# Performance work log

Hardware: AMD Instinct MI355X
Metric: run time of the kernel (lower is better)

The kernel has to match this reference:

```python
import jax, jax.numpy as jnp
import numpy as np

B, M, P, A, T = 32, 128, 20, 32, 32
H = 32   # embed_size / local hidden
E = 64   # local_hidden_dim = 2*H, global attention embed dim


def setup_inputs() -> dict:
    key = jax.random.key(0)
    ks = jax.random.split(key, 10)
    def w(k, shape, fan):
        return jax.random.normal(k, shape, jnp.float32) / np.float32(np.sqrt(fan))
    z = lambda *s: jnp.zeros(s, jnp.float32)
    o = lambda *s: jnp.ones(s, jnp.float32)
    return {
        "map_states": jax.random.normal(ks[0], (B, M, P, 16), jnp.float32),
        "agent_states": jax.random.normal(ks[1], (B, A, T, 4), jnp.float32),
        "m_W1": w(ks[2], (16, H), 16), "m_b1": z(H), "m_g1": o(H), "m_be1": z(H),
        "m_W2": w(ks[3], (H, H), H),   "m_b2": z(H), "m_g2": o(H), "m_be2": z(H),
        "a_W1": w(ks[4], (4, H), 4),   "a_b1": z(H), "a_g1": o(H), "a_be1": z(H),
        "a_W2": w(ks[5], (H, H), H),   "a_b2": z(H), "a_g2": o(H), "a_be2": z(H),
        # stacked attention params: index 0 = a2m, 1 = agent(self), 2 = m2a
        "att_Wq": w(ks[6], (3, E, E), E), "att_bq": z(3, E),
        "att_Wk": w(ks[7], (3, E, E), E), "att_bk": z(3, E),
        "att_Wv": w(ks[8], (3, E, E), E), "att_bv": z(3, E),
        "att_Wo": w(ks[9], (3, E, E), E), "att_bo": z(3, E),
    }


def _mlp(x, W, b, g, be):
    # Linear -> LayerNorm -> ReLU
    h = x @ W + b
    mu = jnp.mean(h, axis=-1, keepdims=True)
    var = jnp.var(h, axis=-1, keepdims=True)
    h = (h - mu) / jnp.sqrt(var + 1e-5) * g + be
    return jax.nn.relu(h)


def _local_graph(x, p1, p2):
    # x: [B, N, P, F] -> [B, N, 2H]
    e = _mlp(_mlp(x, *p1), *p2)                       # [B,N,P,H]
    n = e.shape[2]
    # faithful "max excluding self": max_j (e[j] - 10000*[j==i])
    mask = -10000.0 * jnp.eye(n, dtype=e.dtype)       # [Pi,Pj]
    nb = jnp.max(e[:, :, None, :, :] + mask[None, None, :, :, None], axis=3)  # [B,N,P,H]
    e = jnp.concatenate([e, nb], axis=-1)             # [B,N,P,2H]
    return jnp.max(e, axis=2)                          # [B,N,2H]


def _mha(q, k, v, Wq, bq, Wk, bk, Wv, bv, Wo, bo):
    # single-head attention, batch_first
    d = q.shape[-1]
    Q = q @ Wq + bq
    K = k @ Wk + bk
    V = v @ Wv + bv
    scores = jnp.einsum('bqd,bkd->bqk', Q, K) / jnp.sqrt(jnp.asarray(d, Q.dtype))
    attn = jax.nn.softmax(scores, axis=-1)
    return jnp.einsum('bqk,bkd->bqd', attn, V) @ Wo + bo


def reference(map_states, agent_states,
              m_W1, m_b1, m_g1, m_be1, m_W2, m_b2, m_g2, m_be2,
              a_W1, a_b1, a_g1, a_be1, a_W2, a_b2, a_g2, a_be2,
              att_Wq, att_bq, att_Wk, att_bk, att_Wv, att_bv, att_Wo, att_bo):
    map_emb = _local_graph(map_states, (m_W1, m_b1, m_g1, m_be1), (m_W2, m_b2, m_g2, m_be2))      # [B,M,E]
    agent_emb = _local_graph(agent_states, (a_W1, a_b1, a_g1, a_be1), (a_W2, a_b2, a_g2, a_be2))  # [B,A,E]

    target = agent_emb[:, :1]                                       # [B,1,E]
    kv = jnp.concatenate([target, map_emb], axis=1)                 # [B,M+1,E]
    a2m = _mha(map_emb, kv, kv, att_Wq[0], att_bq[0], att_Wk[0], att_bk[0],
               att_Wv[0], att_bv[0], att_Wo[0], att_bo[0])
    map_emb = map_emb + a2m
    t_a = _mha(target, target, target, att_Wq[1], att_bq[1], att_Wk[1], att_bk[1],
               att_Wv[1], att_bv[1], att_Wo[1], att_bo[1])
    t_m2a = _mha(target, map_emb, map_emb, att_Wq[2], att_bq[2], att_Wk[2], att_bk[2],
                 att_Wv[2], att_bv[2], att_Wo[2], att_bo[2])
    target = t_a + t_m2a                                            # [B,1,E]
    # pack (target_agent_embedding, map_embedding) into one array [B, M+1, E]
    return jnp.concatenate([target, map_emb], axis=1)
```

## Files before the change

kernel.cpp:

```cpp
#include <hip/hip_runtime.h>

#define BB 32
#define MM 128
#define PP 20
#define AA 32
#define TT 32
#define HH 32
#define EE 64

__device__ __forceinline__ float4 matvec64(const float* __restrict__ W,
                                           const float* __restrict__ xrow,
                                           int s, int t)
{
    const float4* __restrict__ Wv = (const float4*)W;
    const float4* __restrict__ xv = (const float4*)xrow;
    float4 acc = make_float4(0.f, 0.f, 0.f, 0.f);
#pragma unroll
    for (int ii = 0; ii < 4; ++ii) {
        const float4 xx = xv[s * 4 + ii];
        const int ib = s * 16 + ii * 4;
        const float4 w0 = Wv[(ib + 0) * 16 + t];
        const float4 w1 = Wv[(ib + 1) * 16 + t];
        const float4 w2 = Wv[(ib + 2) * 16 + t];
        const float4 w3 = Wv[(ib + 3) * 16 + t];
        acc.x = fmaf(xx.x, w0.x, acc.x); acc.y = fmaf(xx.x, w0.y, acc.y);
        acc.z = fmaf(xx.x, w0.z, acc.z); acc.w = fmaf(xx.x, w0.w, acc.w);
        acc.x = fmaf(xx.y, w1.x, acc.x); acc.y = fmaf(xx.y, w1.y, acc.y);
        acc.z = fmaf(xx.y, w1.z, acc.z); acc.w = fmaf(xx.y, w1.w, acc.w);
        acc.x = fmaf(xx.z, w2.x, acc.x); acc.y = fmaf(xx.z, w2.y, acc.y);
        acc.z = fmaf(xx.z, w2.z, acc.z); acc.w = fmaf(xx.z, w2.w, acc.w);
        acc.x = fmaf(xx.w, w3.x, acc.x); acc.y = fmaf(xx.w, w3.y, acc.y);
        acc.z = fmaf(xx.w, w3.z, acc.z); acc.w = fmaf(xx.w, w3.w, acc.w);
    }
    acc.x += __shfl_xor(acc.x, 16); acc.y += __shfl_xor(acc.y, 16);
    acc.z += __shfl_xor(acc.z, 16); acc.w += __shfl_xor(acc.w, 16);
    acc.x += __shfl_xor(acc.x, 32); acc.y += __shfl_xor(acc.y, 32);
    acc.z += __shfl_xor(acc.z, 32); acc.w += __shfl_xor(acc.w, 32);
    return acc;
}

template <int IN, int P>
__device__ __forceinline__ void lg_qkv_body(const float* __restrict__ xg,
                                            const float* __restrict__ W1, const float* __restrict__ b1,
                                            const float* __restrict__ g1, const float* __restrict__ be1,
                                            const float* __restrict__ W2, const float* __restrict__ b2,
                                            const float* __restrict__ g2, const float* __restrict__ be2,
                                            float* __restrict__ embRow,
                                            const float* __restrict__ Wq, const float* __restrict__ bq,
                                            const float* __restrict__ Wk, const float* __restrict__ bk,
                                            const float* __restrict__ Wv, const float* __restrict__ bv,
                                            float* __restrict__ Qrow,
                                            float* __restrict__ Krow,
                                            float* __restrict__ Vrow)
{
    constexpr int NPASS = (P + 7) / 8;
    const int tid  = threadIdx.x;
    const int wave = tid >> 6;
    const int lane = tid & 63;
    const int sub  = tid >> 5;
    const int c    = tid & 31;

    __shared__ __align__(16) float aslot[8][32];
    __shared__ __align__(16) float wmax[4][32];
    __shared__ __align__(16) float xrow[EE];

    float4 xr[NPASS][IN / 4];
#pragma unroll
    for (int ps = 0; ps < NPASS; ++ps) {
        int p = ps * 8 + sub;
        if (p > P - 1) p = P - 1;
        const float4* xp4 = (const float4*)(xg + (long)p * IN);
#pragma unroll
        for (int j = 0; j < IN / 4; ++j) xr[ps][j] = xp4[j];
    }

    float w1c[IN];
#pragma unroll
    for (int k = 0; k < IN; ++k) w1c[k] = W1[k * HH + c];
    float w2c[HH];
#pragma unroll
    for (int k = 0; k < HH; ++k) w2c[k] = W2[k * HH + c];
    const float b1c = b1[c], g1c = g1[c], be1c = be1[c];
    const float b2c = b2[c], g2c = g2[c], be2c = be2[c];

    float cmax = -1e30f;

#pragma unroll
    for (int ps = 0; ps < NPASS; ++ps) {
        const bool valid = (ps * 8 + sub) < P;

        float ha = b1c, hb = 0.0f;
#pragma unroll
        for (int j = 0; j < IN / 4; ++j) {
            const float4 xx = xr[ps][j];
            ha = fmaf(xx.x, w1c[4 * j + 0], ha);
            hb = fmaf(xx.y, w1c[4 * j + 1], hb);
            ha = fmaf(xx.z, w1c[4 * j + 2], ha);
            hb = fmaf(xx.w, w1c[4 * j + 3], hb);
        }
        const float h = ha + hb;

        float s1 = h, s2 = h * h;
#pragma unroll
        for (int off = 16; off >= 1; off >>= 1) {
            s1 += __shfl_xor(s1, off, 32);
            s2 += __shfl_xor(s2, off, 32);
        }
        const float mu  = s1 * (1.0f / 32.0f);
        float var = s2 * (1.0f / 32.0f) - mu * mu;
        var = fmaxf(var, 0.0f);
        float a = (h - mu) * rsqrtf(var + 1e-5f) * g1c + be1c;
        a = fmaxf(a, 0.0f);

        aslot[sub][c] = a;
        const float4* av4 = (const float4*)aslot[sub];
        float h2a = b2c, h2b = 0.0f;
#pragma unroll
        for (int j = 0; j < 8; ++j) {
            const float4 aa = av4[j];
            h2a = fmaf(aa.x, w2c[4 * j + 0], h2a);
            h2b = fmaf(aa.y, w2c[4 * j + 1], h2b);
            h2a = fmaf(aa.z, w2c[4 * j + 2], h2a);
            h2b = fmaf(aa.w, w2c[4 * j + 3], h2b);
        }
        const float h2 = h2a + h2b;

        float t1 = h2, t2 = h2 * h2;
#pragma unroll
        for (int off = 16; off >= 1; off >>= 1) {
            t1 += __shfl_xor(t1, off, 32);
            t2 += __shfl_xor(t2, off, 32);
        }
        const float mu2  = t1 * (1.0f / 32.0f);
        float var2 = t2 * (1.0f / 32.0f) - mu2 * mu2;
        var2 = fmaxf(var2, 0.0f);
        float e = (h2 - mu2) * rsqrtf(var2 + 1e-5f) * g2c + be2c;
        e = fmaxf(e, 0.0f);

        if (valid) cmax = fmaxf(cmax, e);
    }

    cmax = fmaxf(cmax, __shfl_xor(cmax, 32));
    if (lane < 32) wmax[wave][lane] = cmax;
    __syncthreads();

    if (tid < 32) {
        float fin = fmaxf(fmaxf(wmax[0][tid], wmax[1][tid]),
                          fmaxf(wmax[2][tid], wmax[3][tid]));
        xrow[tid]      = fin;
        xrow[tid + 32] = fin;
        embRow[tid]      = fin;
        embRow[tid + 32] = fin;
    }
    __syncthreads();

    const int s = lane >> 4, t = lane & 15;
    if (wave == 0) {
        if (Qrow) {
            float4 q4 = matvec64(Wq, xrow, s, t);
            if (s == 0) {
                const float4 bq4 = ((const float4*)bq)[t];
                float4 qo;
                qo.x = (q4.x + bq4.x) * 0.125f;
                qo.y = (q4.y + bq4.y) * 0.125f;
                qo.z = (q4.z + bq4.z) * 0.125f;
                qo.w = (q4.w + bq4.w) * 0.125f;
                ((float4*)Qrow)[t] = qo;
            }
        }
    } else if (wave == 1) {
        float4 k4 = matvec64(Wk, xrow, s, t);
        if (s == 0) {
            const float4 kb4 = ((const float4*)bk)[t];
            float4 ko;
            ko.x = k4.x + kb4.x; ko.y = k4.y + kb4.y;
            ko.z = k4.z + kb4.z; ko.w = k4.w + kb4.w;
            ((float4*)Krow)[t] = ko;
        }
    } else if (wave == 2) {
        float4 v4 = matvec64(Wv, xrow, s, t);
        if (s == 0) {
            const float4 vb4 = ((const float4*)bv)[t];
            float4 vo;
            vo.x = v4.x + vb4.x; vo.y = v4.y + vb4.y;
            vo.z = v4.z + vb4.z; vo.w = v4.w + vb4.w;
            ((float4*)Vrow)[t] = vo;
        }
    }
}

__global__ __launch_bounds__(256) void lg_qkv_kernel(
                              const float* __restrict__ map_states,
                              const float* __restrict__ agent_states,
                              const float* __restrict__ mW1, const float* __restrict__ mb1,
                              const float* __restrict__ mg1, const float* __restrict__ mbe1,
                              const float* __restrict__ mW2, const float* __restrict__ mb2,
                              const float* __restrict__ mg2, const float* __restrict__ mbe2,
                              const float* __restrict__ aW1, const float* __restrict__ ab1,
                              const float* __restrict__ ag1, const float* __restrict__ abe1,
                              const float* __restrict__ aW2, const float* __restrict__ ab2,
                              const float* __restrict__ ag2, const float* __restrict__ abe2,
                              const float* __restrict__ Wq, const float* __restrict__ bq,
                              const float* __restrict__ Wk, const float* __restrict__ bk,
                              const float* __restrict__ Wv, const float* __restrict__ bv,
                              float* __restrict__ map_emb,
                              float* __restrict__ target,
                              float* __restrict__ Qb,
                              float* __restrict__ Kb,
                              float* __restrict__ Vb)
{
    const int g = blockIdx.x;
    if (g < BB * MM) {
        const int b = g >> 7, m = g & 127;
        lg_qkv_body<16, PP>(map_states + (long)g * PP * 16,
                        mW1, mb1, mg1, mbe1, mW2, mb2, mg2, mbe2,
                        map_emb + (long)g * EE,
                        Wq, bq, Wk, bk, Wv, bv,
                        Qb + (long)g * EE,
                        Kb + ((long)b * 129 + 1 + m) * EE,
                        Vb + ((long)b * 129 + 1 + m) * EE);
    } else {
        const int b = g - BB * MM;
        lg_qkv_body<4, TT>(agent_states + (long)b * AA * TT * 4,
                       aW1, ab1, ag1, abe1, aW2, ab2, ag2, abe2,
                       target + (long)b * EE,
                       Wq, bq, Wk, bk, Wv, bv,
                       nullptr,
                       Kb + (long)b * 129 * EE,
                       Vb + (long)b * 129 * EE);
    }
}

__global__ void attn_fused_kernel(const float* __restrict__ map_emb,
                                  const float* __restrict__ Qb,
                                  const float* __restrict__ Kb,
                                  const float* __restrict__ Vb,
                                  const float* __restrict__ Wo, const float* __restrict__ bo,
                                  const float* __restrict__ Wk2, const float* __restrict__ bk2,
                                  const float* __restrict__ Wv2, const float* __restrict__ bv2,
                                  float* __restrict__ K2,
                                  float* __restrict__ V2,
                                  float* __restrict__ out)
{
    const int blk  = blockIdx.x;
    const int b    = blk >> 7;
    const int q    = blk & 127;
    const int lane = threadIdx.x;
    const int s = lane >> 4, t = lane & 15;

    __shared__ __align__(16) float sc[132];
    __shared__ __align__(16) float av[EE];
    __shared__ __align__(16) float resrow[EE];

    const float4 q4 = ((const float4*)(Qb + ((long)b * MM + q) * EE))[t];

    const float* Kbase = Kb + (long)b * 129 * EE;
    float mx = -1e30f;
#pragma unroll 4
    for (int it = 0; it < 33; ++it) {
        const int j = it * 4 + s;
        const bool valid = (j < 129);
        float p = 0.0f;
        if (valid) {
            const float4 k4 = ((const float4*)(Kbase + (long)j * EE))[t];
            p = q4.x * k4.x + q4.y * k4.y + q4.z * k4.z + q4.w * k4.w;
        }
        p += __shfl_xor(p, 1); p += __shfl_xor(p, 2);
        p += __shfl_xor(p, 4); p += __shfl_xor(p, 8);
        if (valid) {
            mx = fmaxf(mx, p);
            if (t == 0) sc[j] = p;
        }
    }
#pragma unroll
    for (int off = 32; off >= 1; off >>= 1) mx = fmaxf(mx, __shfl_xor(mx, off));
    __syncthreads();

    float sum = 0.0f;
    for (int j = lane; j < 129; j += 64) {
        const float e = __expf(sc[j] - mx);
        sc[j] = e;
        sum += e;
    }
#pragma unroll
    for (int off = 32; off >= 1; off >>= 1) sum += __shfl_xor(sum, off);
    const float inv = 1.0f / sum;
    __syncthreads();

    const float* Vbase = Vb + (long)b * 129 * EE;
    float4 a4 = make_float4(0.f, 0.f, 0.f, 0.f);
#pragma unroll 4
    for (int it = 0; it < 33; ++it) {
        const int j = it * 4 + s;
        if (j < 129) {
            const float w = sc[j];
            const float4 v4 = ((const float4*)(Vbase + (long)j * EE))[t];
            a4.x = fmaf(w, v4.x, a4.x); a4.y = fmaf(w, v4.y, a4.y);
            a4.z = fmaf(w, v4.z, a4.z); a4.w = fmaf(w, v4.w, a4.w);
        }
    }
    a4.x += __shfl_xor(a4.x, 16); a4.y += __shfl_xor(a4.y, 16);
    a4.z += __shfl_xor(a4.z, 16); a4.w += __shfl_xor(a4.w, 16);
    a4.x += __shfl_xor(a4.x, 32); a4.y += __shfl_xor(a4.y, 32);
    a4.z += __shfl_xor(a4.z, 32); a4.w += __shfl_xor(a4.w, 32);
    if (s == 0) {
        float4 o; o.x = a4.x * inv; o.y = a4.y * inv; o.z = a4.z * inv; o.w = a4.w * inv;
        ((float4*)av)[t] = o;
    }
    __syncthreads();

    const float4 o4 = matvec64(Wo, av, s, t);
    const float4 bo4 = ((const float4*)bo)[t];
    const float4 x4 = ((const float4*)(map_emb + ((long)b * MM + q) * EE))[t];
    float4 res;
    res.x = o4.x + bo4.x + x4.x;
    res.y = o4.y + bo4.y + x4.y;
    res.z = o4.z + bo4.z + x4.z;
    res.w = o4.w + bo4.w + x4.w;
    if (s == 0) {
        ((float4*)(out + ((long)b * 129 + 1 + q) * EE))[t] = res;
        ((float4*)resrow)[t] = res;
    }
    __syncthreads();

    const float4 k4 = matvec64(Wk2, resrow, s, t);
    const float4 v4 = matvec64(Wv2, resrow, s, t);
    if (s == 0) {
        const float4 kb4 = ((const float4*)bk2)[t];
        const float4 vb4 = ((const float4*)bv2)[t];
        float4 ko, vo;
        ko.x = k4.x + kb4.x; ko.y = k4.y + kb4.y; ko.z = k4.z + kb4.z; ko.w = k4.w + kb4.w;
        vo.x = v4.x + vb4.x; vo.y = v4.y + vb4.y; vo.z = v4.z + vb4.z; vo.w = v4.w + vb4.w;
        ((float4*)(K2 + ((long)b * MM + q) * EE))[t] = ko;
        ((float4*)(V2 + ((long)b * MM + q) * EE))[t] = vo;
    }
}

__global__ void target_kernel(const float* __restrict__ target,
                              const float* __restrict__ K2, const float* __restrict__ V2,
                              const float* __restrict__ Wq2, const float* __restrict__ bq2,
                              const float* __restrict__ Wo2, const float* __restrict__ bo2,
                              const float* __restrict__ Wv1, const float* __restrict__ bv1,
                              const float* __restrict__ Wo1, const float* __restrict__ bo1,
                              float* __restrict__ out)
{
    const int b    = blockIdx.x;
    const int lane = threadIdx.x;
    const int s = lane >> 4, t = lane & 15;

    __shared__ __align__(16) float trow[EE];
    __shared__ __align__(16) float tmp[EE];
    __shared__ __align__(16) float sc[128];
    __shared__ __align__(16) float av[EE];

    trow[lane] = target[(long)b * EE + lane];
    __syncthreads();

    const float4 v1 = matvec64(Wv1, trow, s, t);
    if (s == 0) {
        const float4 bv4 = ((const float4*)bv1)[t];
        float4 w; w.x = v1.x + bv4.x; w.y = v1.y + bv4.y; w.z = v1.z + bv4.z; w.w = v1.w + bv4.w;
        ((float4*)tmp)[t] = w;
    }
    __syncthreads();
    float4 ta = matvec64(Wo1, tmp, s, t);
    {
        const float4 bo4 = ((const float4*)bo1)[t];
        ta.x += bo4.x; ta.y += bo4.y; ta.z += bo4.z; ta.w += bo4.w;
    }

    float4 q4 = matvec64(Wq2, trow, s, t);
    {
        const float4 bq4 = ((const float4*)bq2)[t];
        q4.x = (q4.x + bq4.x) * 0.125f;
        q4.y = (q4.y + bq4.y) * 0.125f;
        q4.z = (q4.z + bq4.z) * 0.125f;
        q4.w = (q4.w + bq4.w) * 0.125f;
    }

    const float* Kbase = K2 + (long)b * MM * EE;
    float mx = -1e30f;
#pragma unroll 4
    for (int it = 0; it < 32; ++it) {
        const int j = it * 4 + s;
        const float4 k4 = ((const float4*)(Kbase + (long)j * EE))[t];
        float p = q4.x * k4.x + q4.y * k4.y + q4.z * k4.z + q4.w * k4.w;
        p += __shfl_xor(p, 1); p += __shfl_xor(p, 2);
        p += __shfl_xor(p, 4); p += __shfl_xor(p, 8);
        mx = fmaxf(mx, p);
        if (t == 0) sc[j] = p;
    }
#pragma unroll
    for (int off = 32; off >= 1; off >>= 1) mx = fmaxf(mx, __shfl_xor(mx, off));
    __syncthreads();

    float sum = 0.0f;
#pragma unroll
    for (int j = lane; j < MM; j += 64) {
        const float e = __expf(sc[j] - mx);
        sc[j] = e;
        sum += e;
    }
#pragma unroll
    for (int off = 32; off >= 1; off >>= 1) sum += __shfl_xor(sum, off);
    const float inv = 1.0f / sum;
    __syncthreads();

    const float* Vbase = V2 + (long)b * MM * EE;
    float4 b4 = make_float4(0.f, 0.f, 0.f, 0.f);
#pragma unroll 4
    for (int it = 0; it < 32; ++it) {
        const int j = it * 4 + s;
        const float w = sc[j];
        const float4 vv = ((const float4*)(Vbase + (long)j * EE))[t];
        b4.x = fmaf(w, vv.x, b4.x); b4.y = fmaf(w, vv.y, b4.y);
        b4.z = fmaf(w, vv.z, b4.z); b4.w = fmaf(w, vv.w, b4.w);
    }
    b4.x += __shfl_xor(b4.x, 16); b4.y += __shfl_xor(b4.y, 16);
    b4.z += __shfl_xor(b4.z, 16); b4.w += __shfl_xor(b4.w, 16);
    b4.x += __shfl_xor(b4.x, 32); b4.y += __shfl_xor(b4.y, 32);
    b4.z += __shfl_xor(b4.z, 32); b4.w += __shfl_xor(b4.w, 32);
    if (s == 0) {
        float4 o; o.x = b4.x * inv; o.y = b4.y * inv; o.z = b4.z * inv; o.w = b4.w * inv;
        ((float4*)av)[t] = o;
    }
    __syncthreads();

    const float4 o4 = matvec64(Wo2, av, s, t);
    if (s == 0) {
        const float4 bo4 = ((const float4*)bo2)[t];
        float4 r;
        r.x = ta.x + o4.x + bo4.x;
        r.y = ta.y + o4.y + bo4.y;
        r.z = ta.z + o4.z + bo4.z;
        r.w = ta.w + o4.w + bo4.w;
        ((float4*)(out + (long)b * 129 * EE))[t] = r;
    }
}

extern "C" void kernel_launch(void* const* d_in, const int* in_sizes, int n_in,
                              void* d_out, int out_size, void* d_ws, size_t ws_size,
                              hipStream_t stream)
{
    const float* map_states   = (const float*)d_in[0];
    const float* agent_states = (const float*)d_in[1];
    const float* m_W1 = (const float*)d_in[2];
    const float* m_b1 = (const float*)d_in[3];
    const float* m_g1 = (const float*)d_in[4];
    const float* m_be1 = (const float*)d_in[5];
    const float* m_W2 = (const float*)d_in[6];
    const float* m_b2 = (const float*)d_in[7];
    const float* m_g2 = (const float*)d_in[8];
    const float* m_be2 = (const float*)d_in[9];
    const float* a_W1 = (const float*)d_in[10];
    const float* a_b1 = (const float*)d_in[11];
    const float* a_g1 = (const float*)d_in[12];
    const float* a_be1 = (const float*)d_in[13];
    const float* a_W2 = (const float*)d_in[14];
    const float* a_b2 = (const float*)d_in[15];
    const float* a_g2 = (const float*)d_in[16];
    const float* a_be2 = (const float*)d_in[17];
    const float* att_Wq = (const float*)d_in[18];
    const float* att_bq = (const float*)d_in[19];
    const float* att_Wk = (const float*)d_in[20];
    const float* att_bk = (const float*)d_in[21];
    const float* att_Wv = (const float*)d_in[22];
    const float* att_bv = (const float*)d_in[23];
    const float* att_Wo = (const float*)d_in[24];
    const float* att_bo = (const float*)d_in[25];

    float* out = (float*)d_out;

    float* ws      = (float*)d_ws;
    float* map_emb = ws;
    float* target  = map_emb + BB * MM * EE;
    float* Qb      = target + BB * EE;
    float* Kb      = Qb + BB * MM * EE;
    float* Vb      = Kb + BB * 129 * EE;
    float* K2      = Vb + BB * 129 * EE;
    float* V2      = K2 + BB * MM * EE;

    const float* Wq0 = att_Wq + 0 * EE * EE; const float* bq0 = att_bq + 0 * EE;
    const float* Wk0 = att_Wk + 0 * EE * EE; const float* bk0 = att_bk + 0 * EE;
    const float* Wv0 = att_Wv + 0 * EE * EE; const float* bv0 = att_bv + 0 * EE;
    const float* Wo0 = att_Wo + 0 * EE * EE; const float* bo0 = att_bo + 0 * EE;
    const float* Wv1 = att_Wv + 1 * EE * EE; const float* bv1 = att_bv + 1 * EE;
    const float* Wo1 = att_Wo + 1 * EE * EE; const float* bo1 = att_bo + 1 * EE;
    const float* Wq2 = att_Wq + 2 * EE * EE; const float* bq2 = att_bq + 2 * EE;
    const float* Wk2 = att_Wk + 2 * EE * EE; const float* bk2 = att_bk + 2 * EE;
    const float* Wv2 = att_Wv + 2 * EE * EE; const float* bv2 = att_bv + 2 * EE;
    const float* Wo2 = att_Wo + 2 * EE * EE; const float* bo2 = att_bo + 2 * EE;

    hipLaunchKernelGGL(lg_qkv_kernel, dim3(BB * MM + BB), dim3(256), 0, stream,
                       map_states, agent_states,
                       m_W1, m_b1, m_g1, m_be1, m_W2, m_b2, m_g2, m_be2,
                       a_W1, a_b1, a_g1, a_be1, a_W2, a_b2, a_g2, a_be2,
                       Wq0, bq0, Wk0, bk0, Wv0, bv0,
                       map_emb, target, Qb, Kb, Vb);

    hipLaunchKernelGGL(attn_fused_kernel, dim3(BB * MM), dim3(64), 0, stream,
                       map_emb, Qb, Kb, Vb, Wo0, bo0,
                       Wk2, bk2, Wv2, bv2, K2, V2, out);

    hipLaunchKernelGGL(target_kernel, dim3(BB), dim3(64), 0, stream,
                       target, K2, V2, Wq2, bq2, Wo2, bo2, Wv1, bv1, Wo1, bo1, out);
}
```

Measured before the change: 180.0 us.

## Fold m2a key/value projections into the target query and attention output

The per-map-row K2/V2 projections for the m2a attention are no longer computed. The target kernel instead projects the query through Wk2 (q·K = (q·Wk2ᵀ)·r, with the key bias dropped because it is constant across keys under softmax). It then applies Wv2 plus bias after the weighted sum of the residual rows, since the softmax weights sum to one. This removes two 64x64 matvecs per map row, an extra barrier, and the K2/V2 workspace traffic from the large attention kernel. In exchange the small 32-block target kernel does a little more serial work and reads the map rows directly from the output buffer.

```diff
diff --git a/kernel.cpp b/kernel.cpp
--- a/kernel.cpp
+++ b/kernel.cpp
@@ -236,10 +236,6 @@
                                   const float* __restrict__ Kb,
                                   const float* __restrict__ Vb,
                                   const float* __restrict__ Wo, const float* __restrict__ bo,
-                                  const float* __restrict__ Wk2, const float* __restrict__ bk2,
-                                  const float* __restrict__ Wv2, const float* __restrict__ bv2,
-                                  float* __restrict__ K2,
-                                  float* __restrict__ V2,
                                   float* __restrict__ out)
 {
     const int blk  = blockIdx.x;
@@ -250,7 +246,6 @@
 
     __shared__ __align__(16) float sc[132];
     __shared__ __align__(16) float av[EE];
-    __shared__ __align__(16) float resrow[EE];
 
     const float4 q4 = ((const float4*)(Qb + ((long)b * MM + q) * EE))[t];
 
@@ -310,35 +305,22 @@
     __syncthreads();
 
     const float4 o4 = matvec64(Wo, av, s, t);
-    const float4 bo4 = ((const float4*)bo)[t];
-    const float4 x4 = ((const float4*)(map_emb + ((long)b * MM + q) * EE))[t];
-    float4 res;
-    res.x = o4.x + bo4.x + x4.x;
-    res.y = o4.y + bo4.y + x4.y;
-    res.z = o4.z + bo4.z + x4.z;
-    res.w = o4.w + bo4.w + x4.w;
-    if (s == 0) {
+    if (s == 0) {
+        const float4 bo4 = ((const float4*)bo)[t];
+        const float4 x4 = ((const float4*)(map_emb + ((long)b * MM + q) * EE))[t];
+        float4 res;
+        res.x = o4.x + bo4.x + x4.x;
+        res.y = o4.y + bo4.y + x4.y;
+        res.z = o4.z + bo4.z + x4.z;
+        res.w = o4.w + bo4.w + x4.w;
         ((float4*)(out + ((long)b * 129 + 1 + q) * EE))[t] = res;
-        ((float4*)resrow)[t] = res;
-    }
-    __syncthreads();
-
-    const float4 k4 = matvec64(Wk2, resrow, s, t);
-    const float4 v4 = matvec64(Wv2, resrow, s, t);
-    if (s == 0) {
-        const float4 kb4 = ((const float4*)bk2)[t];
-        const float4 vb4 = ((const float4*)bv2)[t];
-        float4 ko, vo;
-        ko.x = k4.x + kb4.x; ko.y = k4.y + kb4.y; ko.z = k4.z + kb4.z; ko.w = k4.w + kb4.w;
-        vo.x = v4.x + vb4.x; vo.y = v4.y + vb4.y; vo.z = v4.z + vb4.z; vo.w = v4.w + vb4.w;
-        ((float4*)(K2 + ((long)b * MM + q) * EE))[t] = ko;
-        ((float4*)(V2 + ((long)b * MM + q) * EE))[t] = vo;
     }
 }
 
 __global__ void target_kernel(const float* __restrict__ target,
-                              const float* __restrict__ K2, const float* __restrict__ V2,
                               const float* __restrict__ Wq2, const float* __restrict__ bq2,
+                              const float* __restrict__ Wk2,
+                              const float* __restrict__ Wv2, const float* __restrict__ bv2,
                               const float* __restrict__ Wo2, const float* __restrict__ bo2,
                               const float* __restrict__ Wv1, const float* __restrict__ bv1,
                               const float* __restrict__ Wo1, const float* __restrict__ bo1,
@@ -350,6 +332,8 @@
 
     __shared__ __align__(16) float trow[EE];
     __shared__ __align__(16) float tmp[EE];
+    __shared__ __align__(16) float qtl[EE];
+    __shared__ __align__(16) float qkl[EE];
     __shared__ __align__(16) float sc[128];
     __shared__ __align__(16) float av[EE];
 
@@ -370,21 +354,42 @@
     }
 
     float4 q4 = matvec64(Wq2, trow, s, t);
+    if (s == 0) {
+        const float4 bq4 = ((const float4*)bq2)[t];
+        float4 qo;
+        qo.x = (q4.x + bq4.x) * 0.125f;
+        qo.y = (q4.y + bq4.y) * 0.125f;
+        qo.z = (q4.z + bq4.z) * 0.125f;
+        qo.w = (q4.w + bq4.w) * 0.125f;
+        ((float4*)qtl)[t] = qo;
+    }
+    __syncthreads();
+
     {
-        const float4 bq4 = ((const float4*)bq2)[t];
-        q4.x = (q4.x + bq4.x) * 0.125f;
-        q4.y = (q4.y + bq4.y) * 0.125f;
-        q4.z = (q4.z + bq4.z) * 0.125f;
-        q4.w = (q4.w + bq4.w) * 0.125f;
-    }
-
-    const float* Kbase = K2 + (long)b * MM * EE;
+        const float4* Wrow = (const float4*)(Wk2 + (long)lane * EE);
+        const float4* qt4  = (const float4*)qtl;
+        float qa = 0.f, qb = 0.f;
+#pragma unroll
+        for (int j = 0; j < 16; j += 2) {
+            const float4 w0 = Wrow[j],     x0 = qt4[j];
+            const float4 w1 = Wrow[j + 1], x1 = qt4[j + 1];
+            qa = fmaf(w0.x, x0.x, qa); qb = fmaf(w0.y, x0.y, qb);
+            qa = fmaf(w0.z, x0.z, qa); qb = fmaf(w0.w, x0.w, qb);
+            qa = fmaf(w1.x, x1.x, qa); qb = fmaf(w1.y, x1.y, qb);
+            qa = fmaf(w1.z, x1.z, qa); qb = fmaf(w1.w, x1.w, qb);
+        }
+        qkl[lane] = qa + qb;
+    }
+    __syncthreads();
+
+    const float* Rbase = out + ((long)b * 129 + 1) * EE;
+    const float4 qk4 = ((const float4*)qkl)[t];
     float mx = -1e30f;
 #pragma unroll 4
     for (int it = 0; it < 32; ++it) {
         const int j = it * 4 + s;
-        const float4 k4 = ((const float4*)(Kbase + (long)j * EE))[t];
-        float p = q4.x * k4.x + q4.y * k4.y + q4.z * k4.z + q4.w * k4.w;
+        const float4 r4 = ((const float4*)(Rbase + (long)j * EE))[t];
+        float p = qk4.x * r4.x + qk4.y * r4.y + qk4.z * r4.z + qk4.w * r4.w;
         p += __shfl_xor(p, 1); p += __shfl_xor(p, 2);
         p += __shfl_xor(p, 4); p += __shfl_xor(p, 8);
         mx = fmaxf(mx, p);
@@ -406,15 +411,14 @@
     const float inv = 1.0f / sum;
     __syncthreads();
 
-    const float* Vbase = V2 + (long)b * MM * EE;
     float4 b4 = make_float4(0.f, 0.f, 0.f, 0.f);
 #pragma unroll 4
     for (int it = 0; it < 32; ++it) {
         const int j = it * 4 + s;
         const float w = sc[j];
-        const float4 vv = ((const float4*)(Vbase + (long)j * EE))[t];
-        b4.x = fmaf(w, vv.x, b4.x); b4.y = fmaf(w, vv.y, b4.y);
-        b4.z = fmaf(w, vv.z, b4.z); b4.w = fmaf(w, vv.w, b4.w);
+        const float4 rr = ((const float4*)(Rbase + (long)j * EE))[t];
+        b4.x = fmaf(w, rr.x, b4.x); b4.y = fmaf(w, rr.y, b4.y);
+        b4.z = fmaf(w, rr.z, b4.z); b4.w = fmaf(w, rr.w, b4.w);
     }
     b4.x += __shfl_xor(b4.x, 16); b4.y += __shfl_xor(b4.y, 16);
     b4.z += __shfl_xor(b4.z, 16); b4.w += __shfl_xor(b4.w, 16);
@@ -426,7 +430,15 @@
     }
     __syncthreads();
 
-    const float4 o4 = matvec64(Wo2, av, s, t);
+    const float4 vv = matvec64(Wv2, av, s, t);
+    if (s == 0) {
+        const float4 bv4 = ((const float4*)bv2)[t];
+        float4 w; w.x = vv.x + bv4.x; w.y = vv.y + bv4.y; w.z = vv.z + bv4.z; w.w = vv.w + bv4.w;
+        ((float4*)tmp)[t] = w;
+    }
+    __syncthreads();
+
+    const float4 o4 = matvec64(Wo2, tmp, s, t);
     if (s == 0) {
         const float4 bo4 = ((const float4*)bo2)[t];
         float4 r;
@@ -477,8 +489,6 @@
     float* Qb      = target + BB * EE;
     float* Kb      = Qb + BB * MM * EE;
     float* Vb      = Kb + BB * 129 * EE;
-    float* K2      = Vb + BB * 129 * EE;
-    float* V2      = K2 + BB * MM * EE;
 
     const float* Wq0 = att_Wq + 0 * EE * EE; const float* bq0 = att_bq + 0 * EE;
     const float* Wk0 = att_Wk + 0 * EE * EE; const float* bk0 = att_bk + 0 * EE;
@@ -487,7 +497,7 @@
     const float* Wv1 = att_Wv + 1 * EE * EE; const float* bv1 = att_bv + 1 * EE;
     const float* Wo1 = att_Wo + 1 * EE * EE; const float* bo1 = att_bo + 1 * EE;
     const float* Wq2 = att_Wq + 2 * EE * EE; const float* bq2 = att_bq + 2 * EE;
-    const float* Wk2 = att_Wk + 2 * EE * EE; const float* bk2 = att_bk + 2 * EE;
+    const float* Wk2 = att_Wk + 2 * EE * EE;
     const float* Wv2 = att_Wv + 2 * EE * EE; const float* bv2 = att_bv + 2 * EE;
     const float* Wo2 = att_Wo + 2 * EE * EE; const float* bo2 = att_bo + 2 * EE;
 
@@ -499,9 +509,9 @@
                        map_emb, target, Qb, Kb, Vb);
 
     hipLaunchKernelGGL(attn_fused_kernel, dim3(BB * MM), dim3(64), 0, stream,
-                       map_emb, Qb, Kb, Vb, Wo0, bo0,
-                       Wk2, bk2, Wv2, bv2, K2, V2, out);
+                       map_emb, Qb, Kb, Vb, Wo0, bo0, out);
 
     hipLaunchKernelGGL(target_kernel, dim3(BB), dim3(64), 0, stream,
-                       target, K2, V2, Wq2, bq2, Wo2, bo2, Wv1, bv1, Wo1, bo1, out);
+                       target, Wq2, bq2, Wk2, Wv2, bv2, Wo2, bo2,
+                       Wv1, bv1, Wo1, bo1, out);
 }
```

Result: faster. 176.1 us (-2.1%).
